# Optimization experiments

Hardware: AMD Instinct MI355X
Metric: run time of the kernel (lower is better)

## Reference

```python
import math
import jax, jax.numpy as jnp
import numpy as np

B, C, H, W = 2, 256, 256, 256
TH, TW = 256, 256
U = V = 2            # window_size
PE_DIM = 256
DIM = 256
HEADS = 8
TEMP = 10000.0


def sine_pe(y, x, num_pos_feats, temp, card):
    """Faithful port of get_sine_position_encoding (use_norm=True)."""
    eps = 1e-6
    scale = 2.0 * math.pi
    y = y / (card[0] + eps) * scale
    x = x / (card[1] + eps) * scale
    dt = jnp.arange(num_pos_feats, dtype=jnp.float32)
    dim_t = temp ** (2.0 * jnp.floor(dt / 2.0) / num_pos_feats)
    px = x[..., None] / dim_t
    py = y[..., None] / dim_t

    def interleave(p):
        s = jnp.stack((jnp.sin(p[..., 0::2]), jnp.cos(p[..., 1::2])), axis=-1)
        return s.reshape(s.shape[:-2] + (-1,))

    return jnp.concatenate((interleave(py), interleave(px)), axis=-1)


def setup_inputs() -> dict:
    key = jax.random.key(0)
    ks = jax.random.split(key, 8)
    return {
        "feat_supp": jax.random.normal(ks[0], (B, C, H, W), jnp.float32),
        "offset": jax.random.normal(ks[1], (B, TH, TW, 2), jnp.float32) * 2.0,
        "Wq": jax.random.normal(ks[2], (DIM, PE_DIM), jnp.float32) * 0.02,
        "bq": jax.random.normal(ks[3], (DIM,), jnp.float32) * 0.02,
        "Wk": jax.random.normal(ks[4], (DIM, PE_DIM), jnp.float32) * 0.02,
        "bk": jax.random.normal(ks[5], (DIM,), jnp.float32) * 0.02,
        "Wv": jax.random.normal(ks[6], (DIM, PE_DIM), jnp.float32) * 0.02,
        "bv": jax.random.normal(ks[7], (DIM,), jnp.float32) * 0.02,
    }


def reference(feat_supp, offset, Wq, bq, Wk, bk, Wv, bv):
    UV = U * V
    THW = TH * TW
    Dh = DIM // HEADS
    attn_scale = Dh ** (-0.5)
    d = PE_DIM // C  # = 1 here

    # --- warp grid: integer window corners + fractional residual ---
    tgt = jnp.stack(jnp.meshgrid(jnp.arange(TH), jnp.arange(TW), indexing='ij'), axis=-1)  # [TH,TW,2]
    win = jnp.stack(jnp.meshgrid(jnp.arange(U), jnp.arange(V), indexing='ij'), axis=-1)    # [U,V,2]
    full = tgt[None].astype(jnp.float32) + offset[..., ::-1]            # [B,TH,TW,2]
    intg = jnp.floor(full).astype(jnp.int32)
    deci = (full - intg.astype(full.dtype)).reshape(B, THW, 2)          # fractional part
    idx = (intg[:, :, :, None, None, :] + win[None, None, None]).reshape(B, THW * UV, 2)

    # --- duplicate-padding gather (gather_hw) ---
    h_idx = jnp.clip(idx[..., 0], 0, H - 1)
    w_idx = jnp.clip(idx[..., 1], 0, W - 1)
    feat = feat_supp.transpose(0, 2, 3, 1).reshape(B, H * W, C)
    lin = h_idx * W + w_idx                                             # [B, THW*UV]
    feat_warp = jnp.take_along_axis(feat, lin[:, :, None], axis=1)      # [B, THW*UV, C]
    feat_warp_ori = feat_warp.reshape(B, THW, UV, C, 1)

    # --- sine PE on window coords (card = window_size - 1) ---
    ye, xe = jnp.meshgrid(jnp.arange(U, dtype=jnp.float32), jnp.arange(V, dtype=jnp.float32), indexing='ij')
    pos_bias = sine_pe(ye.reshape(1, -1), xe.reshape(1, -1), PE_DIM // 2, TEMP, (U - 1, V - 1))  # [1,UV,PE_DIM]
    pe_warp = pos_bias.reshape(1, 1, UV, C, d)
    fw = (feat_warp_ori + pe_warp).reshape(B, THW, UV, PE_DIM)

    # --- query features: window mean + sine PE of fractional offset (card = window_size) ---
    feat_base = feat_warp_ori[..., 0].mean(axis=2)                      # [B,THW,C]
    pe_curr = sine_pe(deci[..., 0], deci[..., 1], PE_DIM // 2, TEMP, (U, V)).reshape(B, THW, C, d)
    fb = (feat_base[..., None] + pe_curr).reshape(B, THW, PE_DIM)

    # --- cross attention: 1 query vs UV keys per target pixel ---
    q = (fb @ Wq.T + bq).reshape(B, THW, HEADS, Dh)
    k = (fw @ Wk.T + bk).reshape(B, THW, UV, HEADS, Dh)
    v = (fw @ Wv.T + bv).reshape(B, THW, UV, HEADS, Dh)
    attn = jnp.einsum('bthd,btuhd->bthu', q * attn_scale, k)
    attn = jax.nn.softmax(attn, axis=-1)
    out = jnp.einsum('bthu,btuhd->bthd', attn, v).reshape(B, TH, TW, DIM)
    return out.transpose(0, 3, 1, 2)                                    # [B, DIM, TH, TW]
```

## Files before the change

kernel.cpp:

```cpp
#include <hip/hip_runtime.h>


using short8 = __attribute__((ext_vector_type(8))) short;
using uint4v = __attribute__((ext_vector_type(4))) unsigned;
using f32x4  = __attribute__((ext_vector_type(4))) float;
typedef unsigned short u16;

#define LOG2_1E4 13.287712379549449f
#define TWO_PI   6.283185307179586f
#define ATT_SCL  0.17677669529663687f

__device__ __forceinline__ float bs2f(u16 s) {
    unsigned u = ((unsigned)s) << 16;
    float f; __builtin_memcpy(&f, &u, 4); return f;
}
__device__ __forceinline__ u16 f2bs(float f) {
    unsigned u; __builtin_memcpy(&u, &f, 4);
    u += 0x7fffu + ((u >> 16) & 1u);
    return (u16)(u >> 16);
}
__device__ __forceinline__ unsigned cvt_pk_bf16(float lo, float hi) {
    unsigned r;
    asm("v_cvt_pk_bf16_f32 %0, %1, %2" : "=v"(r) : "v"(lo), "v"(hi));
    return r;
}

__device__ __forceinline__ int probe_is_f32(const u16* offs_raw) {
    const int lane = threadIdx.x & 63;
    const float v = bs2f(offs_raw[lane * 2]);
    const float av = fabsf(v);
    const bool insane = !(av >= 1e-3f && av <= 1000.0f);
    return __popcll(__ballot(insane)) >= 16 ? 1 : 0;
}

__global__ __launch_bounds__(256) void irm_canon(
    const void* offs_raw, const void* Wq_r, const void* bq_r,
    const void* Wk_r, const void* bk_r, const void* Wv_r, const void* bv_r,
    unsigned char* canon)
{
    const int is_f32 = probe_is_f32((const u16*)offs_raw);
    float* offsC = (float*)canon;
    u16* WqC = (u16*)(canon + (1u << 20));
    u16* WkC = (u16*)(canon + (1u << 20) + (1u << 17));
    u16* WvC = (u16*)(canon + (1u << 20) + (2u << 17));
    u16* bqC = (u16*)(canon + (1u << 20) + (3u << 17));
    u16* bkC = bqC + 256;
    u16* bvC = bkC + 256;

    const int gid = blockIdx.x * 256 + threadIdx.x;
    if (gid < 262144) {
        offsC[gid] = is_f32 ? ((const float*)offs_raw)[gid]
                            : bs2f(((const u16*)offs_raw)[gid]);
    } else if (gid < 262144 + 3 * 65536) {
        const int r = gid - 262144, w = r >> 16, i = r & 65535;
        const void* src = (w == 0) ? Wq_r : (w == 1) ? Wk_r : Wv_r;
        u16*       dst  = (w == 0) ? WqC  : (w == 1) ? WkC  : WvC;
        dst[i] = is_f32 ? f2bs(((const float*)src)[i]) : ((const u16*)src)[i];
    } else if (gid < 262144 + 3 * 65536 + 3 * 256) {
        const int r = gid - 262144 - 3 * 65536, w = r >> 8, i = r & 255;
        const void* src = (w == 0) ? bq_r : (w == 1) ? bk_r : bv_r;
        u16*       dst  = (w == 0) ? bqC  : (w == 1) ? bkC  : bvC;
        dst[i] = is_f32 ? f2bs(((const float*)src)[i]) : ((const u16*)src)[i];
    }
}

__global__ __launch_bounds__(256) void irm_transpose(const void* __restrict__ feat_raw,
                                                     const u16* __restrict__ offs_raw,
                                                     u16* __restrict__ featT) {
    const int is_f32 = probe_is_f32(offs_raw);
    __shared__ u16 tile[64][72];
    const int b   = blockIdx.z;
    const int c0  = blockIdx.y << 6;
    const int hw0 = blockIdx.x << 6;
    const int tid = threadIdx.x;
    const int r    = tid >> 4;
    const int col4 = (tid & 15) << 2;
    #pragma unroll
    for (int it = 0; it < 4; ++it) {
        const int c = (it << 4) + r;
        const size_t idx = ((size_t)((b << 8) + c0 + c) << 16) + hw0 + col4;
        ushort4 o;
        if (is_f32) {
            const float4 v = *(const float4*)((const float*)feat_raw + idx);
            const unsigned lo = cvt_pk_bf16(v.x, v.y);
            const unsigned hi = cvt_pk_bf16(v.z, v.w);
            o.x = (u16)(lo & 0xffffu); o.y = (u16)(lo >> 16);
            o.z = (u16)(hi & 0xffffu); o.w = (u16)(hi >> 16);
        } else {
            o = *(const ushort4*)((const u16*)feat_raw + idx);
        }
        *(ushort4*)&tile[c][col4 ^ (((c >> 3) & 7) << 3)] = o;
    }
    __syncthreads();
    const int s = tid & 7;
    const int m = tid >> 3;
    #pragma unroll
    for (int it2 = 0; it2 < 2; ++it2) {
        const int hw = (it2 << 5) + m;
        short8 o;
        #pragma unroll
        for (int k = 0; k < 8; ++k) {
            const int c = (s << 3) + k;
            o[k] = (short)tile[c][hw ^ (((c >> 3) & 7) << 3)];
        }
        u16* dst = featT + (((size_t)((b << 16) + hw0 + hw)) << 8) + c0 + (s << 3);
        *(short8*)dst = o;
    }
}

__global__ __launch_bounds__(256, 3) void irm_main(
    const void* __restrict__ fsrc,
    const int transposed,
    const u16* __restrict__ offs_raw,
    const float* __restrict__ offsC,
    const u16* __restrict__ Wq, const u16* __restrict__ bq,
    const u16* __restrict__ Wk, const u16* __restrict__ bk_unused,
    const u16* __restrict__ Wv, const u16* __restrict__ bv,
    void* __restrict__ out_raw)
{
    const int is_f32 = probe_is_f32(offs_raw);

    __shared__ __align__(16) unsigned char smem[40960];
    u16* sFb = (u16*)smem;
    u16* sFw = (u16*)(smem + 8192);

    const int tid = threadIdx.x;
    const int raw = blockIdx.x;
    const int wq_ = ((raw & 7) << 10) | (raw >> 3);
    const int b   = wq_ >> 12;
    const int t0  = (wq_ & 4095) << 4;

    const int lane = tid & 63;
    const int wv   = tid >> 6;
    const int c15  = lane & 15;
    const int qd   = lane >> 4;
    const int colbase = wv << 6;

    const int p0 = tid >> 4;
    const int cx = tid & 15;
    const int t  = t0 + p0;
    const float offx = offsC[((((size_t)b << 16) + (size_t)t) << 1) + 0];
    const float offy = offsC[((((size_t)b << 16) + (size_t)t) << 1) + 1];

    short8 pfKa[8];

    {
        const int ty = t >> 8, tx = t & 255;
        const float fy = (float)ty + offy;
        const float fx = (float)tx + offx;
        const float fiy = floorf(fy), fix = floorf(fx);
        const int iy = (int)fiy, ix = (int)fix;
        const float dy = fy - fiy, dx = fx - fix;

        int lin4[4];
        #pragma unroll
        for (int u = 0; u < 4; ++u) {
            int hy = iy + (u >> 1); hy = hy < 0 ? 0 : (hy > 255 ? 255 : hy);
            int wx = ix + (u & 1);  wx = wx < 0 ? 0 : (wx > 255 ? 255 : wx);
            lin4[u] = (hy << 8) | wx;
        }

        short8 g[4][2];
        if (transposed) {
            #pragma unroll
            for (int u = 0; u < 4; ++u) {
                const u16* src = (const u16*)fsrc +
                    ((((size_t)(b << 16)) + (size_t)lin4[u]) << 8) + (cx << 4);
                g[u][0] = *(const short8*)(src);
                g[u][1] = *(const short8*)(src + 8);
            }
        } else {
            #pragma unroll
            for (int u = 0; u < 4; ++u) {
                #pragma unroll
                for (int i = 0; i < 8; ++i) {
                    const size_t i0 = (((size_t)((b << 8) + (cx << 4) + i)) << 16) + lin4[u];
                    const size_t i1 = (((size_t)((b << 8) + (cx << 4) + 8 + i)) << 16) + lin4[u];
                    g[u][0][i] = is_f32 ? (short)f2bs(((const float*)fsrc)[i0]) : (short)((const u16*)fsrc)[i0];
                    g[u][1][i] = is_f32 ? (short)f2bs(((const float*)fsrc)[i1]) : (short)((const u16*)fsrc)[i1];
                }
            }
        }

        float invt[8], s1[8], c1[8];
        #pragma unroll
        for (int a = 0; a < 8; ++a) {
            const int j = ((cx << 3) + a) & 63;
            invt[a] = exp2f(-(float)j * (LOG2_1E4 / 64.0f));
            const float arg = (TWO_PI / (1.0f + 1e-6f)) * invt[a];
            __sincosf(arg, &s1[a], &c1[a]);
        }

        const bool hi_half = (cx >= 8);
        float gsum[16];
        #pragma unroll
        for (int i = 0; i < 16; ++i) gsum[i] = 0.0f;

        #pragma unroll
        for (int u = 0; u < 4; ++u) {
            const bool sel = hi_half ? (bool)(u & 1) : (bool)(u >> 1);
            unsigned pk[8];
            #pragma unroll
            for (int a = 0; a < 8; ++a) {
                const float f0 = bs2f((u16)g[u][a >> 2][(2 * a) & 7]);
                const float f1 = bs2f((u16)g[u][a >> 2][(2 * a + 1) & 7]);
                gsum[2 * a]     += f0;
                gsum[2 * a + 1] += f1;
                const float w0 = f0 + (sel ? s1[a] : 0.0f);
                const float w1 = f1 + (sel ? c1[a] : 1.0f);
                pk[a] = cvt_pk_bf16(w0, w1);
            }
            const int row = (p0 << 2) + u;
            const int rp  = row ^ (((row >> 3) ^ cx) & 7);
            const uint4v lo = {pk[0], pk[1], pk[2], pk[3]};
            const uint4v hi = {pk[4], pk[5], pk[6], pk[7]};
            *(uint4v*)&sFw[(((2 * cx) * 64 + rp)) * 8]     = lo;
            *(uint4v*)&sFw[(((2 * cx + 1) * 64 + rp)) * 8] = hi;
        }

        #pragma unroll
        for (int ks = 0; ks < 8; ++ks)
            pfKa[ks] = *(const short8*)&Wk[(colbase + c15) * 256 + ks * 32 + qd * 8];

        const float ys = dy * (TWO_PI / (2.0f + 1e-6f));
        const float xs = dx * (TWO_PI / (2.0f + 1e-6f));
        const float sxy = hi_half ? xs : ys;
        unsigned qk[8];
        #pragma unroll
        for (int a = 0; a < 8; ++a) {
            float s2, c2;
            __sincosf(sxy * invt[a], &s2, &c2);
            qk[a] = cvt_pk_bf16(gsum[2 * a] * 0.25f + s2, gsum[2 * a + 1] * 0.25f + c2);
        }
        const int rb = p0 ^ (cx & 7);
        const uint4v qlo = {qk[0], qk[1], qk[2], qk[3]};
        const uint4v qhi = {qk[4], qk[5], qk[6], qk[7]};
        *(uint4v*)&sFb[((2 * cx) * 16 + rb) * 8]     = qlo;
        *(uint4v*)&sFb[((2 * cx + 1) * 16 + rb) * 8] = qhi;
    }
    __syncthreads();

    const f32x4 zero4 = {0.f, 0.f, 0.f, 0.f};
    const int krow0 = 4 * c15;
    const int kw_hi = (c15 >> 1) & 7;

    #pragma unroll
    for (int h2 = 0; h2 < 2; ++h2) {
        const int ntA = 2 * h2, ntB = 2 * h2 + 1;
        __builtin_amdgcn_sched_barrier(0);

        short8 wb[8], pfQ[8];
        #pragma unroll
        for (int ks = 0; ks < 8; ++ks)
            wb[ks] = *(const short8*)&Wk[(colbase + ntB * 16 + c15) * 256 + ks * 32 + qd * 8];
        #pragma unroll
        for (int ks = 0; ks < 8; ++ks)
            pfQ[ks] = *(const short8*)&Wq[(colbase + ntA * 16 + c15) * 256 + ks * 32 + qd * 8];
        f32x4 accT[4][2];
        #pragma unroll
        for (int u = 0; u < 4; ++u) { accT[u][0] = zero4; accT[u][1] = zero4; }
        #pragma unroll
        for (int ks = 0; ks < 8; ++ks) {
            const int gk = ((ks * 4 + qd) >> 1) & 7;
            #pragma unroll
            for (int u = 0; u < 4; ++u) {
                const int rr = (krow0 + u) ^ (kw_hi ^ gk);
                const short8 bf = *(const short8*)&sFw[((ks * 4 + qd) * 64 + rr) * 8];
                accT[u][0] = __builtin_amdgcn_mfma_f32_16x16x32_bf16(pfKa[ks], bf, accT[u][0], 0, 0, 0);
                accT[u][1] = __builtin_amdgcn_mfma_f32_16x16x32_bf16(wb[ks],   bf, accT[u][1], 0, 0, 0);
            }
        }
        __builtin_amdgcn_sched_barrier(0);

        short8 qb[8], pfV[8];
        #pragma unroll
        for (int ks = 0; ks < 8; ++ks)
            qb[ks] = *(const short8*)&Wq[(colbase + ntB * 16 + c15) * 256 + ks * 32 + qd * 8];
        #pragma unroll
        for (int ks = 0; ks < 8; ++ks)
            pfV[ks] = *(const short8*)&Wv[(colbase + ntA * 16 + c15) * 256 + ks * 32 + qd * 8];
        f32x4 accQ[2] = {zero4, zero4};
        #pragma unroll
        for (int ks = 0; ks < 8; ++ks) {
            const int gidx = ks * 4 + qd;
            const short8 bfb = *(const short8*)&sFb[(gidx * 16 + (c15 ^ ((gidx >> 1) & 7))) * 8];
            accQ[0] = __builtin_amdgcn_mfma_f32_16x16x32_bf16(pfQ[ks], bfb, accQ[0], 0, 0, 0);
            accQ[1] = __builtin_amdgcn_mfma_f32_16x16x32_bf16(qb[ks],  bfb, accQ[1], 0, 0, 0);
        }
        {
            const ushort4 b40 = *(const ushort4*)&bq[colbase + ntA * 16 + qd * 4];
            const ushort4 b41 = *(const ushort4*)&bq[colbase + ntB * 16 + qd * 4];
            accQ[0][0] += bs2f(b40.x); accQ[0][1] += bs2f(b40.y);
            accQ[0][2] += bs2f(b40.z); accQ[0][3] += bs2f(b40.w);
            accQ[1][0] += bs2f(b41.x); accQ[1][1] += bs2f(b41.y);
            accQ[1][2] += bs2f(b41.z); accQ[1][3] += bs2f(b41.w);
        }
        __builtin_amdgcn_sched_barrier(0);

        float att[4];
        {
            float lg[4];
            #pragma unroll
            for (int u = 0; u < 4; ++u) {
                float acc = 0.0f;
                #pragma unroll
                for (int ntl = 0; ntl < 2; ++ntl)
                    #pragma unroll
                    for (int r = 0; r < 4; ++r)
                        acc += accQ[ntl][r] * accT[u][ntl][r];
                acc += __shfl_xor(acc, 16);
                acc += __shfl_xor(acc, 32);
                lg[u] = acc * ATT_SCL;
            }
            const float mx = fmaxf(fmaxf(lg[0], lg[1]), fmaxf(lg[2], lg[3]));
            float e[4], es = 0.0f;
            #pragma unroll
            for (int u = 0; u < 4; ++u) { e[u] = __expf(lg[u] - mx); es += e[u]; }
            const float inv = __fdividef(1.0f, es);
            #pragma unroll
            for (int u = 0; u < 4; ++u) att[u] = e[u] * inv;
        }
        __builtin_amdgcn_sched_barrier(0);

        short8 vb[8];
        #pragma unroll
        for (int ks = 0; ks < 8; ++ks)
            vb[ks] = *(const short8*)&Wv[(colbase + ntB * 16 + c15) * 256 + ks * 32 + qd * 8];
        if (h2 == 0) {
            #pragma unroll
            for (int ks = 0; ks < 8; ++ks)
                pfKa[ks] = *(const short8*)&Wk[(colbase + 32 + c15) * 256 + ks * 32 + qd * 8];
        }
        #pragma unroll
        for (int u = 0; u < 4; ++u) { accT[u][0] = zero4; accT[u][1] = zero4; }
        #pragma unroll
        for (int ks = 0; ks < 8; ++ks) {
            const int gk = ((ks * 4 + qd) >> 1) & 7;
            #pragma unroll
            for (int u = 0; u < 4; ++u) {
                const int rr = (krow0 + u) ^ (kw_hi ^ gk);
                const short8 bf = *(const short8*)&sFw[((ks * 4 + qd) * 64 + rr) * 8];
                accT[u][0] = __builtin_amdgcn_mfma_f32_16x16x32_bf16(pfV[ks], bf, accT[u][0], 0, 0, 0);
                accT[u][1] = __builtin_amdgcn_mfma_f32_16x16x32_bf16(vb[ks],  bf, accT[u][1], 0, 0, 0);
            }
        }
        __builtin_amdgcn_sched_barrier(0);

        #pragma unroll
        for (int ntl = 0; ntl < 2; ++ntl) {
            const int nt = 2 * h2 + ntl;
            const ushort4 bv4 = *(const ushort4*)&bv[colbase + nt * 16 + qd * 4];
            const float bvf[4] = {bs2f(bv4.x), bs2f(bv4.y), bs2f(bv4.z), bs2f(bv4.w)};
            const int cbase = (b << 8) + colbase + nt * 16 + qd * 4;
            #pragma unroll
            for (int r = 0; r < 4; ++r) {
                float val = att[0] * accT[0][ntl][r];
                val += att[1] * accT[1][ntl][r];
                val += att[2] * accT[2][ntl][r];
                val += att[3] * accT[3][ntl][r];
                val += bvf[r];
                if (is_f32) {
                    ((float*)out_raw)[(((size_t)(cbase + r)) << 16) + t0 + c15] = val;
                } else {
                    ((u16*)out_raw)[(((size_t)(cbase + r)) << 16) + t0 + c15] = f2bs(val);
                }
            }
        }
    }
}

extern "C" void kernel_launch(void* const* d_in, const int* in_sizes, int n_in,
                              void* d_out, int out_size, void* d_ws, size_t ws_size,
                              hipStream_t stream) {
    const size_t FEATT_BYTES = (size_t)1 << 26;
    const size_t CANON_BYTES = (1u << 20) + (3u << 17) + 3 * 512;
    const int use_t = (ws_size >= FEATT_BYTES + CANON_BYTES) ? 1 : 0;

    unsigned char* ws    = (unsigned char*)d_ws;
    unsigned char* canon = ws + (use_t ? FEATT_BYTES : 0);
    float* offsC = (float*)canon;
    u16* WqC = (u16*)(canon + (1u << 20));
    u16* WkC = (u16*)(canon + (1u << 20) + (1u << 17));
    u16* WvC = (u16*)(canon + (1u << 20) + (2u << 17));
    u16* bqC = (u16*)(canon + (1u << 20) + (3u << 17));
    u16* bkC = bqC + 256;
    u16* bvC = bkC + 256;

    irm_canon<<<1795, 256, 0, stream>>>(d_in[1], d_in[2], d_in[3], d_in[4],
                                        d_in[5], d_in[6], d_in[7], canon);
    if (use_t)
        irm_transpose<<<dim3(1024, 4, 2), 256, 0, stream>>>(d_in[0], (const u16*)d_in[1], (u16*)ws);
    irm_main<<<dim3(8192), 256, 0, stream>>>(use_t ? (const void*)ws : d_in[0], use_t,
                                             (const u16*)d_in[1], offsC,
                                             WqC, bqC, WkC, bkC, WvC, bvC, d_out);
}
```

Before: 685.9 us.

## Drop weight prefetch pipeline, load weights in half-K chunks for higher occupancy

Removes the cross-phase register prefetching of Wk/Wq/Wv fragments. Each projection GEMM now loads its weight fragments in two half-K chunks of 8 short8 registers just before use. Launch bounds rise from 3 to 4 waves-per-EU to cut register pressure and increase occupancy. The trade is that weight-load latency is no longer hidden behind the previous MFMA phase and must instead be covered by more resident waves.

```diff
diff --git a/kernel.cpp b/kernel.cpp
--- a/kernel.cpp
+++ b/kernel.cpp
@@ -108,7 +108,7 @@
     }
 }
 
-__global__ __launch_bounds__(256, 3) void irm_main(
+__global__ __launch_bounds__(256, 4) void irm_main(
     const void* __restrict__ fsrc,
     const int transposed,
     const u16* __restrict__ offs_raw,
@@ -142,8 +142,6 @@
     const float offx = offsC[((((size_t)b << 16) + (size_t)t) << 1) + 0];
     const float offy = offsC[((((size_t)b << 16) + (size_t)t) << 1) + 1];
 
-    short8 pfKa[8];
-
     {
         const int ty = t >> 8, tx = t & 255;
         const float fy = (float)ty + offy;
@@ -218,10 +216,6 @@
             *(uint4v*)&sFw[(((2 * cx + 1) * 64 + rp)) * 8] = hi;
         }
 
-        #pragma unroll
-        for (int ks = 0; ks < 8; ++ks)
-            pfKa[ks] = *(const short8*)&Wk[(colbase + c15) * 256 + ks * 32 + qd * 8];
-
         const float ys = dy * (TWO_PI / (2.0f + 1e-6f));
         const float xs = dx * (TWO_PI / (2.0f + 1e-6f));
         const float sxy = hi_half ? xs : ys;
@@ -247,45 +241,26 @@
     #pragma unroll
     for (int h2 = 0; h2 < 2; ++h2) {
         const int ntA = 2 * h2, ntB = 2 * h2 + 1;
-        __builtin_amdgcn_sched_barrier(0);
-
-        short8 wb[8], pfQ[8];
-        #pragma unroll
-        for (int ks = 0; ks < 8; ++ks)
-            wb[ks] = *(const short8*)&Wk[(colbase + ntB * 16 + c15) * 256 + ks * 32 + qd * 8];
-        #pragma unroll
-        for (int ks = 0; ks < 8; ++ks)
-            pfQ[ks] = *(const short8*)&Wq[(colbase + ntA * 16 + c15) * 256 + ks * 32 + qd * 8];
-        f32x4 accT[4][2];
-        #pragma unroll
-        for (int u = 0; u < 4; ++u) { accT[u][0] = zero4; accT[u][1] = zero4; }
-        #pragma unroll
-        for (int ks = 0; ks < 8; ++ks) {
-            const int gk = ((ks * 4 + qd) >> 1) & 7;
-            #pragma unroll
-            for (int u = 0; u < 4; ++u) {
-                const int rr = (krow0 + u) ^ (kw_hi ^ gk);
-                const short8 bf = *(const short8*)&sFw[((ks * 4 + qd) * 64 + rr) * 8];
-                accT[u][0] = __builtin_amdgcn_mfma_f32_16x16x32_bf16(pfKa[ks], bf, accT[u][0], 0, 0, 0);
-                accT[u][1] = __builtin_amdgcn_mfma_f32_16x16x32_bf16(wb[ks],   bf, accT[u][1], 0, 0, 0);
-            }
-        }
-        __builtin_amdgcn_sched_barrier(0);
-
-        short8 qb[8], pfV[8];
-        #pragma unroll
-        for (int ks = 0; ks < 8; ++ks)
-            qb[ks] = *(const short8*)&Wq[(colbase + ntB * 16 + c15) * 256 + ks * 32 + qd * 8];
-        #pragma unroll
-        for (int ks = 0; ks < 8; ++ks)
-            pfV[ks] = *(const short8*)&Wv[(colbase + ntA * 16 + c15) * 256 + ks * 32 + qd * 8];
+
         f32x4 accQ[2] = {zero4, zero4};
         #pragma unroll
-        for (int ks = 0; ks < 8; ++ks) {
-            const int gidx = ks * 4 + qd;
-            const short8 bfb = *(const short8*)&sFb[(gidx * 16 + (c15 ^ ((gidx >> 1) & 7))) * 8];
-            accQ[0] = __builtin_amdgcn_mfma_f32_16x16x32_bf16(pfQ[ks], bfb, accQ[0], 0, 0, 0);
-            accQ[1] = __builtin_amdgcn_mfma_f32_16x16x32_bf16(qb[ks],  bfb, accQ[1], 0, 0, 0);
+        for (int half = 0; half < 2; ++half) {
+            short8 wf[8];
+            #pragma unroll
+            for (int i = 0; i < 8; ++i) {
+                const int ks = half * 4 + (i >> 1);
+                const int nt = (i & 1) ? ntB : ntA;
+                wf[i] = *(const short8*)&Wq[(colbase + nt * 16 + c15) * 256 + ks * 32 + qd * 8];
+            }
+            #pragma unroll
+            for (int k4 = 0; k4 < 4; ++k4) {
+                const int ks = half * 4 + k4;
+                const int gidx = ks * 4 + qd;
+                const short8 bfb = *(const short8*)&sFb[(gidx * 16 + (c15 ^ ((gidx >> 1) & 7))) * 8];
+                accQ[0] = __builtin_amdgcn_mfma_f32_16x16x32_bf16(wf[k4 * 2 + 0], bfb, accQ[0], 0, 0, 0);
+                accQ[1] = __builtin_amdgcn_mfma_f32_16x16x32_bf16(wf[k4 * 2 + 1], bfb, accQ[1], 0, 0, 0);
+            }
+            __builtin_amdgcn_sched_barrier(0);
         }
         {
             const ushort4 b40 = *(const ushort4*)&bq[colbase + ntA * 16 + qd * 4];
@@ -295,7 +270,33 @@
             accQ[1][0] += bs2f(b41.x); accQ[1][1] += bs2f(b41.y);
             accQ[1][2] += bs2f(b41.z); accQ[1][3] += bs2f(b41.w);
         }
-        __builtin_amdgcn_sched_barrier(0);
+
+        f32x4 accT[4][2];
+        #pragma unroll
+        for (int u = 0; u < 4; ++u) { accT[u][0] = zero4; accT[u][1] = zero4; }
+        #pragma unroll
+        for (int half = 0; half < 2; ++half) {
+            short8 wf[8];
+            #pragma unroll
+            for (int i = 0; i < 8; ++i) {
+                const int ks = half * 4 + (i >> 1);
+                const int nt = (i & 1) ? ntB : ntA;
+                wf[i] = *(const short8*)&Wk[(colbase + nt * 16 + c15) * 256 + ks * 32 + qd * 8];
+            }
+            #pragma unroll
+            for (int k4 = 0; k4 < 4; ++k4) {
+                const int ks = half * 4 + k4;
+                const int gk = ((ks * 4 + qd) >> 1) & 7;
+                #pragma unroll
+                for (int u = 0; u < 4; ++u) {
+                    const int rr = (krow0 + u) ^ (kw_hi ^ gk);
+                    const short8 bf = *(const short8*)&sFw[((ks * 4 + qd) * 64 + rr) * 8];
+                    accT[u][0] = __builtin_amdgcn_mfma_f32_16x16x32_bf16(wf[k4 * 2 + 0], bf, accT[u][0], 0, 0, 0);
+                    accT[u][1] = __builtin_amdgcn_mfma_f32_16x16x32_bf16(wf[k4 * 2 + 1], bf, accT[u][1], 0, 0, 0);
+                }
+            }
+            __builtin_amdgcn_sched_barrier(0);
+        }
 
         float att[4];
         {
@@ -322,29 +323,31 @@
         }
         __builtin_amdgcn_sched_barrier(0);
 
-        short8 vb[8];
-        #pragma unroll
-        for (int ks = 0; ks < 8; ++ks)
-            vb[ks] = *(const short8*)&Wv[(colbase + ntB * 16 + c15) * 256 + ks * 32 + qd * 8];
-        if (h2 == 0) {
-            #pragma unroll
-            for (int ks = 0; ks < 8; ++ks)
-                pfKa[ks] = *(const short8*)&Wk[(colbase + 32 + c15) * 256 + ks * 32 + qd * 8];
-        }
         #pragma unroll
         for (int u = 0; u < 4; ++u) { accT[u][0] = zero4; accT[u][1] = zero4; }
         #pragma unroll
-        for (int ks = 0; ks < 8; ++ks) {
-            const int gk = ((ks * 4 + qd) >> 1) & 7;
-            #pragma unroll
-            for (int u = 0; u < 4; ++u) {
-                const int rr = (krow0 + u) ^ (kw_hi ^ gk);
-                const short8 bf = *(const short8*)&sFw[((ks * 4 + qd) * 64 + rr) * 8];
-                accT[u][0] = __builtin_amdgcn_mfma_f32_16x16x32_bf16(pfV[ks], bf, accT[u][0], 0, 0, 0);
-                accT[u][1] = __builtin_amdgcn_mfma_f32_16x16x32_bf16(vb[ks],  bf, accT[u][1], 0, 0, 0);
-            }
-        }
-        __builtin_amdgcn_sched_barrier(0);
+        for (int half = 0; half < 2; ++half) {
+            short8 wf[8];
+            #pragma unroll
+            for (int i = 0; i < 8; ++i) {
+                const int ks = half * 4 + (i >> 1);
+                const int nt = (i & 1) ? ntB : ntA;
+                wf[i] = *(const short8*)&Wv[(colbase + nt * 16 + c15) * 256 + ks * 32 + qd * 8];
+            }
+            #pragma unroll
+            for (int k4 = 0; k4 < 4; ++k4) {
+                const int ks = half * 4 + k4;
+                const int gk = ((ks * 4 + qd) >> 1) & 7;
+                #pragma unroll
+                for (int u = 0; u < 4; ++u) {
+                    const int rr = (krow0 + u) ^ (kw_hi ^ gk);
+                    const short8 bf = *(const short8*)&sFw[((ks * 4 + qd) * 64 + rr) * 8];
+                    accT[u][0] = __builtin_amdgcn_mfma_f32_16x16x32_bf16(wf[k4 * 2 + 0], bf, accT[u][0], 0, 0, 0);
+                    accT[u][1] = __builtin_amdgcn_mfma_f32_16x16x32_bf16(wf[k4 * 2 + 1], bf, accT[u][1], 0, 0, 0);
+                }
+            }
+            __builtin_amdgcn_sched_barrier(0);
+        }
 
         #pragma unroll
         for (int ntl = 0; ntl < 2; ++ntl) {
@@ -366,6 +369,7 @@
                 }
             }
         }
+        __builtin_amdgcn_sched_barrier(0);
     }
 }
 
```

Result: faster. 615.7 us (-10.2%).
